# Kernel optimization log

Hardware: AMD Instinct MI355X
Metric: run time of the kernel (lower is better)

The kernel has to match this reference:

```python
import jax, jax.numpy as jnp
import numpy as np

DIM = 512
NUM_HEADS = 8


def setup_inputs() -> dict:
    key = jax.random.key(0)
    ks = jax.random.split(key, 9)
    B, C, H, W = 8, DIM, 32, 32
    s = 1.0 / np.sqrt(DIM)  # conv-style init scale
    return {
        "x": jax.random.normal(ks[0], (B, C, H, W), jnp.float32),
        "Wq": jax.random.normal(ks[1], (DIM, DIM), jnp.float32) * s,
        "bq": jnp.zeros((DIM,), jnp.float32),
        "Wk": jax.random.normal(ks[2], (DIM, DIM), jnp.float32) * s,
        "bk": jnp.zeros((DIM,), jnp.float32),
        "Wv": jax.random.normal(ks[3], (DIM, DIM), jnp.float32) * s,
        "bv": jnp.zeros((DIM,), jnp.float32),
        "Wo": jax.random.normal(ks[4], (DIM, DIM), jnp.float32) * s,
        "bo": jnp.zeros((DIM,), jnp.float32),
    }


def _proj(x, W, b):
    # 1x1 conv == per-pixel linear over channels: [out_c, in_c] x [b, in_c, h, w]
    return jnp.einsum('oc,bchw->bohw', W, x) + b[None, :, None, None]


def reference(x, Wq, bq, Wk, bk, Wv, bv, Wo, bo):
    b, c, h, w = x.shape
    g = NUM_HEADS
    dh = c // g  # per-head channels
    q = _proj(x, Wq, bq)
    k = _proj(x, Wk, bk)
    v = _proj(x, Wv, bv)
    # 'b (g c) h w -> (b g) c (h w)'
    def split_heads(t):
        return t.reshape(b, g, dh, h * w).reshape(b * g, dh, h * w)
    q, k, v = split_heads(q), split_heads(k), split_heads(v)
    # note: scale uses full dim (as in the source), not per-head dim
    a = jnp.einsum('bcs,bct->bst', q, k) / jnp.sqrt(jnp.float32(c))
    a = jax.nn.softmax(a, axis=-1)  # dropout is identity at inference
    o = jnp.einsum('bst,bct->bcs', a, v)  # [(b g), dh, s]
    o = o.reshape(b, g * dh, h, w)  # '(b g) c (h w) -> b (g c) h w'
    return x + _proj(o, Wo, bo)
```

## Files before the change

kernel.cpp:

```cpp
#include <hip/hip_runtime.h>

typedef unsigned short u16;
typedef __attribute__((ext_vector_type(8))) short short8;
typedef __attribute__((ext_vector_type(4))) short sh4;
typedef __attribute__((ext_vector_type(2))) int int2v;
typedef __attribute__((ext_vector_type(4))) float floatx4;

__device__ __forceinline__ float b2f(u16 u) {
  unsigned int x = ((unsigned int)u) << 16;
  return __builtin_bit_cast(float, x);
}
__device__ __forceinline__ u16 f2b(float f) {
  unsigned int x = __builtin_bit_cast(unsigned int, f);
  unsigned int r = (x + 0x7FFFu + ((x >> 16) & 1u)) >> 16;
  return (u16)r;
}
__device__ __forceinline__ unsigned int pk2bf(float a, float b) {
  unsigned int ua = __builtin_bit_cast(unsigned int, a) + 0x8000u;
  unsigned int ub = __builtin_bit_cast(unsigned int, b) + 0x8000u;
  return __builtin_amdgcn_perm(ub, ua, 0x07060302u);
}

#if __has_builtin(__builtin_amdgcn_mfma_f32_16x16x16bf16_1k)
#define MFMA16(a, b, c) __builtin_amdgcn_mfma_f32_16x16x16bf16_1k((a), (b), (c), 0, 0, 0)
#define MFMA16_DRAIN()
#else
__device__ __forceinline__ floatx4 mfma16_fb(sh4 a, sh4 b, floatx4 c) {
  asm volatile("s_nop 1\n\tv_mfma_f32_16x16x16_bf16 %0, %1, %2, %0"
               : "+v"(c) : "v"(a), "v"(b));
  return c;
}
#define MFMA16(a, b, c) mfma16_fb((a), (b), (c))
#define MFMA16_DRAIN() asm volatile("s_nop 7\n\ts_nop 7\n\ts_nop 7")
#endif

#if __has_builtin(__builtin_amdgcn_exp2f)
#define EXP2F(x) __builtin_amdgcn_exp2f(x)
#else
#define EXP2F(x) __expf((x) * 0.6931471805599453f)
#endif

#define MFMA32(a, b, c) __builtin_amdgcn_mfma_f32_16x16x32_bf16((a), (b), (c), 0, 0, 0)

#define GLL16(g, l) __builtin_amdgcn_global_load_lds(                         \
    (const __attribute__((address_space(1))) unsigned int*)(g),               \
    (__attribute__((address_space(3))) unsigned int*)(l), 16, 0, 0)

#define SC_LOG2E 0.06375872f

__device__ __forceinline__ int detect_fp32(const u16* __restrict__ x) {
  __shared__ int cnt;
  if (threadIdx.x == 0) cnt = 0;
  __syncthreads();
  int c = 0;
  if (threadIdx.x < 256) {
#pragma unroll
    for (int i = 0; i < 16; ++i) {
      u16 u = x[threadIdx.x * 16 + i];
      if (((u >> 7) & 0xFF) >= 0xC8) c++;
    }
  }
  if (c) atomicAdd(&cnt, c);
  __syncthreads();
  return cnt > 32;
}

__global__ __launch_bounds__(256) void prep(
    const u16* __restrict__ x,
    const u16* w0, const u16* w1, const u16* w2, const u16* w3,
    const u16* c0, const u16* c1, const u16* c2, const u16* c3,
    u16* __restrict__ xT, u16* __restrict__ Wc, u16* __restrict__ bc, int b0) {
  const int fp32 = detect_fp32(x);
  const int tid = threadIdx.x;
  if (blockIdx.y < 8) {
    __shared__ u16 t[64][65];
    const int lb = blockIdx.z, b = b0 + lb;
    const int p0 = blockIdx.x * 64, cc0 = blockIdx.y * 64;
    const int tx = tid & 63, ty = tid >> 6;
    if (fp32) {
      const float* xb = (const float*)x + (long)b * 524288;
#pragma unroll
      for (int i = 0; i < 16; ++i) {
        int c = ty + i * 4;
        t[c][tx] = f2b(xb[(long)(cc0 + c) * 1024 + p0 + tx]);
      }
    } else {
      const u16* xb = x + (long)b * 524288;
#pragma unroll
      for (int i = 0; i < 16; ++i) {
        int c = ty + i * 4;
        t[c][tx] = xb[(long)(cc0 + c) * 1024 + p0 + tx];
      }
    }
    __syncthreads();
    u16* xTb = xT + (long)lb * 524288;
#pragma unroll
    for (int i = 0; i < 16; ++i) {
      int p = ty + i * 4;
      xTb[(long)(p0 + p) * 512 + cc0 + tx] = t[tx][p];
    }
  } else {
    const u16* srcs[8] = {w0, w1, w2, w3, c0, c1, c2, c3};
    const int nthreads = gridDim.z * 16 * 256;
    const int flat = (blockIdx.z * 16 + blockIdx.x) * 256 + tid;
    for (int vi = flat; vi < 131072; vi += nthreads) {
      int w = vi >> 15;
      int off = (vi & 32767) * 8;
      u16* dst = Wc + w * 262144 + off;
      if (fp32) {
        const float* s = (const float*)srcs[w] + off;
        u16 tmp[8];
#pragma unroll
        for (int r = 0; r < 8; ++r) tmp[r] = f2b(s[r]);
        *(int4*)dst = *(const int4*)tmp;
      } else {
        *(int4*)dst = *(const int4*)(srcs[w] + off);
      }
    }
    for (int gi = flat; gi < 2048; gi += nthreads) {
      int t2 = gi >> 9;
      bc[gi] = fp32 ? f2b(((const float*)srcs[4 + t2])[gi & 511]) : srcs[4 + t2][gi & 511];
    }
  }
}

struct GemmLds64 {
  u16 As0[128][32], As1[128][32];
  u16 Bs0[128][32], Bs1[128][32];
};

__device__ __forceinline__ void gemm_core64(const u16* __restrict__ A, int lda,
                                            const u16* __restrict__ B, int ldb,
                                            int m0, int n0, int K,
                                            GemmLds64& lds, floatx4 (&acc)[4][4]) {
  const int tid = threadIdx.x;
  const int wave = tid >> 6, lane = tid & 63;
  const int quad = lane >> 4, l15 = lane & 15;
  const int wm = (wave >> 1) * 64, wn = (wave & 1) * 64;
  const int lrow = lane >> 2, lcol = (lane & 3) * 8;
  for (int k0 = 0; k0 < K; k0 += 64) {
    __syncthreads();
#pragma unroll
    for (int it = 0; it < 2; ++it) {
      const int rbase = wave * 32 + it * 16;
      const u16* Ar = A + (long)(m0 + rbase + lrow) * lda + k0 + lcol;
      GLL16(Ar, &lds.As0[rbase][0]);
      GLL16(Ar + 32, &lds.As1[rbase][0]);
      const u16* Br = B + (long)(n0 + rbase + lrow) * ldb + k0 + lcol;
      GLL16(Br, &lds.Bs0[rbase][0]);
      GLL16(Br + 32, &lds.Bs1[rbase][0]);
    }
    __syncthreads();
    short8 af[4], bf[4];
#pragma unroll
    for (int i = 0; i < 4; ++i)
      af[i] = *(const short8*)&lds.As0[wm + i * 16 + l15][quad * 8];
#pragma unroll
    for (int j = 0; j < 4; ++j)
      bf[j] = *(const short8*)&lds.Bs0[wn + j * 16 + l15][quad * 8];
#pragma unroll
    for (int i = 0; i < 4; ++i)
#pragma unroll
      for (int j = 0; j < 4; ++j)
        acc[i][j] = MFMA32(af[i], bf[j], acc[i][j]);
#pragma unroll
    for (int i = 0; i < 4; ++i)
      af[i] = *(const short8*)&lds.As1[wm + i * 16 + l15][quad * 8];
#pragma unroll
    for (int j = 0; j < 4; ++j)
      bf[j] = *(const short8*)&lds.Bs1[wn + j * 16 + l15][quad * 8];
#pragma unroll
    for (int i = 0; i < 4; ++i)
#pragma unroll
      for (int j = 0; j < 4; ++j)
        acc[i][j] = MFMA32(af[i], bf[j], acc[i][j]);
  }
}

__global__ __launch_bounds__(256) void gemm_qkv(
    const u16* __restrict__ xT, const u16* __restrict__ Wc,
    const u16* __restrict__ bc, u16* __restrict__ Qt, u16* __restrict__ Kt,
    u16* __restrict__ Vv) {
  __shared__ GemmLds64 lds;
  const long bz = blockIdx.y;
  const u16* xb = xT + bz * 524288;
  const int bx = blockIdx.x;
  const int qk = bx < 64;
  const int t = qk ? bx : bx - 64;
  const int m0 = (t >> 3) * 128, n0 = (t & 7) * 128;
  const u16* A = qk ? xb : (Wc + 524288);
  const u16* B = qk ? Wc : xb;
  floatx4 acc[4][4] = {};
  gemm_core64(A, 512, B, 512, m0, n0, 512, lds, acc);
  const int lane = threadIdx.x & 63, wave = threadIdx.x >> 6;
  const int quad = lane >> 4, l15 = lane & 15;
  const int wm = (wave >> 1) * 64, wn = (wave & 1) * 64;
  if (qk) {
    u16* Qz = Qt + bz * 524288;
    u16* Kz = Kt + bz * 524288;
#pragma unroll
    for (int i = 0; i < 4; ++i)
#pragma unroll
      for (int j = 0; j < 4; ++j)
#pragma unroll
        for (int r = 0; r < 4; ++r) {
          int gm = m0 + wm + i * 16 + quad * 4 + r;
          int gn = n0 + wn + j * 16 + l15;
          float v = acc[i][j][r] + b2f(bc[gn]);
          if (gn < 512) Qz[(long)gm * 512 + gn] = f2b(v * SC_LOG2E);
          else Kz[(long)gm * 512 + gn - 512] = f2b(v);
        }
  } else {
    u16* Vz = Vv + bz * 524288;
    const u16* bv = bc + 1024;
#pragma unroll
    for (int i = 0; i < 4; ++i)
#pragma unroll
      for (int j = 0; j < 4; ++j)
#pragma unroll
        for (int r = 0; r < 4; ++r) {
          int gm = m0 + wm + i * 16 + quad * 4 + r;
          int gn = n0 + wn + j * 16 + l15;
          float v = acc[i][j][r] + b2f(bv[gm]);
          Vz[(long)gm * 1024 + gn] = f2b(v);
        }
  }
}

struct OutLds64 {
  u16 As0[128][32], As1[128][32];
  u16 Bs0[64][32], Bs1[64][32];
};

__global__ __launch_bounds__(256) void gemm_out(
    const u16* __restrict__ Wo, const u16* __restrict__ bo,
    const u16* __restrict__ Ow, const u16* __restrict__ xraw,
    u16* __restrict__ out) {
  const int fp32 = detect_fp32(xraw);
  __shared__ OutLds64 lds;
  const long bz = blockIdx.z;
  const u16* B = Ow + bz * 524288;
  const int m0 = blockIdx.y * 128, n0 = blockIdx.x * 64;
  const int tid = threadIdx.x;
  const int wave = tid >> 6, lane = tid & 63;
  const int quad = lane >> 4, l15 = lane & 15;
  const int lrow = lane >> 2, lcol = (lane & 3) * 8;

  floatx4 acc[2][4] = {};

  for (int k0 = 0; k0 < 512; k0 += 64) {
    __syncthreads();
    {
      const int ra = wave * 32;
      const u16* A0 = Wo + (long)(m0 + ra + lrow) * 512 + k0 + lcol;
      const u16* A1 = Wo + (long)(m0 + ra + 16 + lrow) * 512 + k0 + lcol;
      GLL16(A0, &lds.As0[ra][0]);
      GLL16(A0 + 32, &lds.As1[ra][0]);
      GLL16(A1, &lds.As0[ra + 16][0]);
      GLL16(A1 + 32, &lds.As1[ra + 16][0]);
      const u16* Br = B + (long)(n0 + wave * 16 + lrow) * 512 + k0 + lcol;
      GLL16(Br, &lds.Bs0[wave * 16][0]);
      GLL16(Br + 32, &lds.Bs1[wave * 16][0]);
    }
    __syncthreads();
#pragma unroll
    for (int i = 0; i < 2; ++i) {
      short8 af = *(const short8*)&lds.As0[wave * 32 + i * 16 + l15][quad * 8];
#pragma unroll
      for (int j = 0; j < 4; ++j) {
        short8 bf = *(const short8*)&lds.Bs0[j * 16 + l15][quad * 8];
        acc[i][j] = MFMA32(af, bf, acc[i][j]);
      }
    }
#pragma unroll
    for (int i = 0; i < 2; ++i) {
      short8 af = *(const short8*)&lds.As1[wave * 32 + i * 16 + l15][quad * 8];
#pragma unroll
      for (int j = 0; j < 4; ++j) {
        short8 bf = *(const short8*)&lds.Bs1[j * 16 + l15][quad * 8];
        acc[i][j] = MFMA32(af, bf, acc[i][j]);
      }
    }
  }

#pragma unroll
  for (int i = 0; i < 2; ++i)
#pragma unroll
    for (int j = 0; j < 4; ++j)
#pragma unroll
      for (int r = 0; r < 4; ++r) {
        int gm = m0 + wave * 32 + i * 16 + quad * 4 + r;
        int gn = n0 + j * 16 + l15;
        float v = acc[i][j][r] + b2f(bo[gm]);
        long idx = bz * 524288 + (long)gm * 1024 + gn;
        if (fp32) {
          v += ((const float*)xraw)[idx];
          ((float*)out)[idx] = v;
        } else {
          v += b2f(xraw[idx]);
          out[idx] = f2b(v);
        }
      }
}

#define AP 72
__global__ __launch_bounds__(512, 4) void attn(
    const u16* __restrict__ Qt, const u16* __restrict__ Kt,
    const u16* __restrict__ V, u16* __restrict__ O) {
  __shared__ alignas(16) u16 Ks[2][64][AP];
  __shared__ alignas(16) u16 Vs[2][64][AP];
  const int bg = blockIdx.x;
  const int lb = bg >> 3, head = bg & 7;
  const int s0 = blockIdx.y * 128;
  const int tid = threadIdx.x;
  const int wave = tid >> 6, lane = tid & 63;
  const int quad = lane >> 4, l15 = lane & 15;

  const u16* Qb = Qt + (long)lb * 524288 + head * 64;
  const u16* Kb = Kt + (long)lb * 524288 + head * 64;
  const u16* Vb = V + (long)(lb * 512 + head * 64) * 1024;
  u16* Ob = O + (long)lb * 524288 + head * 64;

  short8 bq[2];
#pragma unroll
  for (int kk = 0; kk < 2; ++kk)
    bq[kk] = *(const short8*)&Qb[(long)(s0 + wave * 16 + l15) * 512 +
                                 kk * 32 + quad * 8];

  const int r0 = tid >> 3, o0 = (tid & 7) * 8;
  int4 kreg, vreg;
  kreg = *(const int4*)&Kb[(long)r0 * 512 + o0];
  vreg = *(const int4*)&Vb[(long)r0 * 1024 + o0];
  *(int4*)&Ks[0][r0][o0] = kreg;
  *(int4*)&Vs[0][r0][o0] = vreg;

  floatx4 acc[4] = {};
  floatx4 accl = {};
  const sh4 ones = {(short)0x3F80, (short)0x3F80, (short)0x3F80, (short)0x3F80};

  for (int it16 = 0; it16 < 16; ++it16) {
    const int buf = it16 & 1;
    const int t0n = (it16 + 1) * 64;
    if (it16 < 15) {
      kreg = *(const int4*)&Kb[(long)(t0n + r0) * 512 + o0];
      vreg = *(const int4*)&Vb[(long)r0 * 1024 + t0n + o0];
    }
    __syncthreads();

    floatx4 p[4] = {};
#pragma unroll
    for (int kk = 0; kk < 2; ++kk) {
      short8 ak[4];
#pragma unroll
      for (int mi = 0; mi < 4; ++mi)
        ak[mi] = *(const short8*)&Ks[buf][mi * 16 + l15][kk * 32 + quad * 8];
#pragma unroll
      for (int mi = 0; mi < 4; ++mi)
        p[mi] = MFMA32(ak[mi], bq[kk], p[mi]);
    }

    sh4 pk[4];
#pragma unroll
    for (int mi = 0; mi < 4; ++mi) {
      float e0 = EXP2F(p[mi][0]);
      float e1 = EXP2F(p[mi][1]);
      float e2 = EXP2F(p[mi][2]);
      float e3 = EXP2F(p[mi][3]);
      int2v w;
      w.x = (int)pk2bf(e0, e1);
      w.y = (int)pk2bf(e2, e3);
      pk[mi] = __builtin_bit_cast(sh4, w);
    }

#pragma unroll
    for (int mi = 0; mi < 4; ++mi) accl = MFMA16(ones, pk[mi], accl);

#pragma unroll
    for (int mi = 0; mi < 4; ++mi) {
      sh4 av[4];
#pragma unroll
      for (int ci = 0; ci < 4; ++ci)
        av[ci] = *(const sh4*)&Vs[buf][ci * 16 + l15][mi * 16 + quad * 4];
#pragma unroll
      for (int ci = 0; ci < 4; ++ci)
        acc[ci] = MFMA16(av[ci], pk[mi], acc[ci]);
    }

    if (it16 < 15) {
      const int nb = 1 - buf;
      *(int4*)&Ks[nb][r0][o0] = kreg;
      *(int4*)&Vs[nb][r0][o0] = vreg;
    }
  }
  MFMA16_DRAIN();

  const float inv = 1.0f / accl[0];

  u16 (*Os)[AP] = (u16(*)[AP]) & Ks[0][0][0];
  __syncthreads();
#pragma unroll
  for (int ci = 0; ci < 4; ++ci) {
    int2v w;
    w.x = (int)pk2bf(acc[ci][0] * inv, acc[ci][1] * inv);
    w.y = (int)pk2bf(acc[ci][2] * inv, acc[ci][3] * inv);
    *(int2v*)&Os[wave * 16 + l15][ci * 16 + quad * 4] = w;
  }
  __syncthreads();
  {
    const int srow = tid >> 2, c16 = (tid & 3) * 16;
    *(int4*)&Ob[(long)(s0 + srow) * 512 + c16] = *(const int4*)&Os[srow][c16];
    *(int4*)&Ob[(long)(s0 + srow) * 512 + c16 + 8] = *(const int4*)&Os[srow][c16 + 8];
  }
}

extern "C" void kernel_launch(void* const* d_in, const int* in_sizes, int n_in,
                              void* d_out, int out_size, void* d_ws, size_t ws_size,
                              hipStream_t stream) {
  const u16* x  = (const u16*)d_in[0];
  const u16* Wq = (const u16*)d_in[1];
  const u16* bq = (const u16*)d_in[2];
  const u16* Wk = (const u16*)d_in[3];
  const u16* bk = (const u16*)d_in[4];
  const u16* Wv = (const u16*)d_in[5];
  const u16* bv = (const u16*)d_in[6];
  const u16* Wo = (const u16*)d_in[7];
  const u16* bo = (const u16*)d_in[8];
  u16* out = (u16*)d_out;
  u16* ws = (u16*)d_ws;

  const size_t PLAN_A_BYTES = 27267072;

  if (ws_size >= PLAN_A_BYTES) {
    u16* xT = ws;
    u16* Kt = ws + 4194304;
    u16* Vv = ws + 8388608;
    u16* Wc = ws + 12582912;
    u16* bc = ws + 13631488;
    u16* Qt = out;
    u16* Ow = xT;

    prep<<<dim3(16, 9, 8), 256, 0, stream>>>(x, Wq, Wk, Wv, Wo,
                                             bq, bk, bv, bo, xT, Wc, bc, 0);
    gemm_qkv<<<dim3(96, 8), 256, 0, stream>>>(xT, Wc, bc, Qt, Kt, Vv);
    attn<<<dim3(64, 8), 512, 0, stream>>>(Qt, Kt, Vv, Ow);
    gemm_out<<<dim3(16, 4, 8), 256, 0, stream>>>(Wc + 786432, bc + 1536, Ow, x, out);
  } else {
    u16* Ow = ws;
    u16* Kt = ws + 4194304;
    u16* Vv = ws + 6291456;
    u16* Wc = ws + 8388608;
    u16* bc = ws + 9437184;
    u16* Qt = out;

    for (int phase = 0; phase < 2; ++phase) {
      const int b0 = phase * 4;
      u16* xT = Ow + (long)phase * 2097152;
      prep<<<dim3(16, 9, 4), 256, 0, stream>>>(x, Wq, Wk, Wv, Wo,
                                               bq, bk, bv, bo, xT, Wc, bc, b0);
      gemm_qkv<<<dim3(96, 4), 256, 0, stream>>>(xT, Wc, bc, Qt, Kt, Vv);
      attn<<<dim3(32, 8), 512, 0, stream>>>(Qt, Kt, Vv, Ow + (long)b0 * 524288);
    }
    gemm_out<<<dim3(16, 4, 8), 256, 0, stream>>>(Wc + 786432, bc + 1536, Ow, x, out);
  }
}
```

Measured before the change: 162.7 us.

## Halve attention block threads with two query tiles per wave; reorder grid dims

```diff
diff --git a/kernel.cpp b/kernel.cpp
--- a/kernel.cpp
+++ b/kernel.cpp
@@ -182,9 +182,9 @@
     const u16* __restrict__ bc, u16* __restrict__ Qt, u16* __restrict__ Kt,
     u16* __restrict__ Vv) {
   __shared__ GemmLds64 lds;
-  const long bz = blockIdx.y;
+  const long bz = blockIdx.x;
   const u16* xb = xT + bz * 524288;
-  const int bx = blockIdx.x;
+  const int bx = blockIdx.y;
   const int qk = bx < 64;
   const int t = qk ? bx : bx - 64;
   const int m0 = (t >> 3) * 128, n0 = (t & 7) * 128;
@@ -238,9 +238,9 @@
     u16* __restrict__ out) {
   const int fp32 = detect_fp32(xraw);
   __shared__ OutLds64 lds;
-  const long bz = blockIdx.z;
+  const long bz = blockIdx.x;
   const u16* B = Ow + bz * 524288;
-  const int m0 = blockIdx.y * 128, n0 = blockIdx.x * 64;
+  const int m0 = blockIdx.z * 128, n0 = blockIdx.y * 64;
   const int tid = threadIdx.x;
   const int wave = tid >> 6, lane = tid & 63;
   const int quad = lane >> 4, l15 = lane & 15;
@@ -304,7 +304,7 @@
 }
 
 #define AP 72
-__global__ __launch_bounds__(512, 4) void attn(
+__global__ __launch_bounds__(256, 2) void attn(
     const u16* __restrict__ Qt, const u16* __restrict__ Kt,
     const u16* __restrict__ V, u16* __restrict__ O) {
   __shared__ alignas(16) u16 Ks[2][64][AP];
@@ -321,33 +321,41 @@
   const u16* Vb = V + (long)(lb * 512 + head * 64) * 1024;
   u16* Ob = O + (long)lb * 524288 + head * 64;
 
-  short8 bq[2];
-#pragma unroll
-  for (int kk = 0; kk < 2; ++kk)
-    bq[kk] = *(const short8*)&Qb[(long)(s0 + wave * 16 + l15) * 512 +
-                                 kk * 32 + quad * 8];
+  short8 bq[2][2];
+#pragma unroll
+  for (int qb = 0; qb < 2; ++qb)
+#pragma unroll
+    for (int kk = 0; kk < 2; ++kk)
+      bq[qb][kk] = *(const short8*)&Qb[(long)(s0 + wave * 32 + qb * 16 + l15) * 512 +
+                                       kk * 32 + quad * 8];
 
   const int r0 = tid >> 3, o0 = (tid & 7) * 8;
-  int4 kreg, vreg;
-  kreg = *(const int4*)&Kb[(long)r0 * 512 + o0];
-  vreg = *(const int4*)&Vb[(long)r0 * 1024 + o0];
-  *(int4*)&Ks[0][r0][o0] = kreg;
-  *(int4*)&Vs[0][r0][o0] = vreg;
-
-  floatx4 acc[4] = {};
-  floatx4 accl = {};
+  int4 kreg0, kreg1, vreg0, vreg1;
+  kreg0 = *(const int4*)&Kb[(long)r0 * 512 + o0];
+  kreg1 = *(const int4*)&Kb[(long)(r0 + 32) * 512 + o0];
+  vreg0 = *(const int4*)&Vb[(long)r0 * 1024 + o0];
+  vreg1 = *(const int4*)&Vb[(long)(r0 + 32) * 1024 + o0];
+  *(int4*)&Ks[0][r0][o0] = kreg0;
+  *(int4*)&Ks[0][r0 + 32][o0] = kreg1;
+  *(int4*)&Vs[0][r0][o0] = vreg0;
+  *(int4*)&Vs[0][r0 + 32][o0] = vreg1;
+
+  floatx4 acc[2][4] = {};
+  floatx4 accl[2] = {};
   const sh4 ones = {(short)0x3F80, (short)0x3F80, (short)0x3F80, (short)0x3F80};
 
   for (int it16 = 0; it16 < 16; ++it16) {
     const int buf = it16 & 1;
     const int t0n = (it16 + 1) * 64;
     if (it16 < 15) {
-      kreg = *(const int4*)&Kb[(long)(t0n + r0) * 512 + o0];
-      vreg = *(const int4*)&Vb[(long)r0 * 1024 + t0n + o0];
-    }
-    __syncthreads();
-
-    floatx4 p[4] = {};
+      kreg0 = *(const int4*)&Kb[(long)(t0n + r0) * 512 + o0];
+      kreg1 = *(const int4*)&Kb[(long)(t0n + r0 + 32) * 512 + o0];
+      vreg0 = *(const int4*)&Vb[(long)r0 * 1024 + t0n + o0];
+      vreg1 = *(const int4*)&Vb[(long)(r0 + 32) * 1024 + t0n + o0];
+    }
+    __syncthreads();
+
+    floatx4 p[2][4] = {};
 #pragma unroll
     for (int kk = 0; kk < 2; ++kk) {
       short8 ak[4];
@@ -355,25 +363,31 @@
       for (int mi = 0; mi < 4; ++mi)
         ak[mi] = *(const short8*)&Ks[buf][mi * 16 + l15][kk * 32 + quad * 8];
 #pragma unroll
-      for (int mi = 0; mi < 4; ++mi)
-        p[mi] = MFMA32(ak[mi], bq[kk], p[mi]);
-    }
-
-    sh4 pk[4];
-#pragma unroll
-    for (int mi = 0; mi < 4; ++mi) {
-      float e0 = EXP2F(p[mi][0]);
-      float e1 = EXP2F(p[mi][1]);
-      float e2 = EXP2F(p[mi][2]);
-      float e3 = EXP2F(p[mi][3]);
-      int2v w;
-      w.x = (int)pk2bf(e0, e1);
-      w.y = (int)pk2bf(e2, e3);
-      pk[mi] = __builtin_bit_cast(sh4, w);
-    }
-
-#pragma unroll
-    for (int mi = 0; mi < 4; ++mi) accl = MFMA16(ones, pk[mi], accl);
+      for (int qb = 0; qb < 2; ++qb)
+#pragma unroll
+        for (int mi = 0; mi < 4; ++mi)
+          p[qb][mi] = MFMA32(ak[mi], bq[qb][kk], p[qb][mi]);
+    }
+
+    sh4 pk[2][4];
+#pragma unroll
+    for (int qb = 0; qb < 2; ++qb)
+#pragma unroll
+      for (int mi = 0; mi < 4; ++mi) {
+        float e0 = EXP2F(p[qb][mi][0]);
+        float e1 = EXP2F(p[qb][mi][1]);
+        float e2 = EXP2F(p[qb][mi][2]);
+        float e3 = EXP2F(p[qb][mi][3]);
+        int2v w;
+        w.x = (int)pk2bf(e0, e1);
+        w.y = (int)pk2bf(e2, e3);
+        pk[qb][mi] = __builtin_bit_cast(sh4, w);
+      }
+
+#pragma unroll
+    for (int qb = 0; qb < 2; ++qb)
+#pragma unroll
+      for (int mi = 0; mi < 4; ++mi) accl[qb] = MFMA16(ones, pk[qb][mi], accl[qb]);
 
 #pragma unroll
     for (int mi = 0; mi < 4; ++mi) {
@@ -382,34 +396,44 @@
       for (int ci = 0; ci < 4; ++ci)
         av[ci] = *(const sh4*)&Vs[buf][ci * 16 + l15][mi * 16 + quad * 4];
 #pragma unroll
-      for (int ci = 0; ci < 4; ++ci)
-        acc[ci] = MFMA16(av[ci], pk[mi], acc[ci]);
+      for (int qb = 0; qb < 2; ++qb)
+#pragma unroll
+        for (int ci = 0; ci < 4; ++ci)
+          acc[qb][ci] = MFMA16(av[ci], pk[qb][mi], acc[qb][ci]);
     }
 
     if (it16 < 15) {
       const int nb = 1 - buf;
-      *(int4*)&Ks[nb][r0][o0] = kreg;
-      *(int4*)&Vs[nb][r0][o0] = vreg;
+      *(int4*)&Ks[nb][r0][o0] = kreg0;
+      *(int4*)&Ks[nb][r0 + 32][o0] = kreg1;
+      *(int4*)&Vs[nb][r0][o0] = vreg0;
+      *(int4*)&Vs[nb][r0 + 32][o0] = vreg1;
     }
   }
   MFMA16_DRAIN();
 
-  const float inv = 1.0f / accl[0];
+  const float inv0 = 1.0f / accl[0][0];
+  const float inv1 = 1.0f / accl[1][0];
 
   u16 (*Os)[AP] = (u16(*)[AP]) & Ks[0][0][0];
   __syncthreads();
 #pragma unroll
-  for (int ci = 0; ci < 4; ++ci) {
-    int2v w;
-    w.x = (int)pk2bf(acc[ci][0] * inv, acc[ci][1] * inv);
-    w.y = (int)pk2bf(acc[ci][2] * inv, acc[ci][3] * inv);
-    *(int2v*)&Os[wave * 16 + l15][ci * 16 + quad * 4] = w;
+  for (int qb = 0; qb < 2; ++qb) {
+    const float inv = qb ? inv1 : inv0;
+#pragma unroll
+    for (int ci = 0; ci < 4; ++ci) {
+      int2v w;
+      w.x = (int)pk2bf(acc[qb][ci][0] * inv, acc[qb][ci][1] * inv);
+      w.y = (int)pk2bf(acc[qb][ci][2] * inv, acc[qb][ci][3] * inv);
+      *(int2v*)&Os[wave * 32 + qb * 16 + l15][ci * 16 + quad * 4] = w;
+    }
   }
   __syncthreads();
   {
-    const int srow = tid >> 2, c16 = (tid & 3) * 16;
-    *(int4*)&Ob[(long)(s0 + srow) * 512 + c16] = *(const int4*)&Os[srow][c16];
-    *(int4*)&Ob[(long)(s0 + srow) * 512 + c16 + 8] = *(const int4*)&Os[srow][c16 + 8];
+    const int srow = tid >> 1, cb = (tid & 1) * 32;
+#pragma unroll
+    for (int c = 0; c < 32; c += 8)
+      *(int4*)&Ob[(long)(s0 + srow) * 512 + cb + c] = *(const int4*)&Os[srow][cb + c];
   }
 }
 
@@ -441,9 +465,9 @@
 
     prep<<<dim3(16, 9, 8), 256, 0, stream>>>(x, Wq, Wk, Wv, Wo,
                                              bq, bk, bv, bo, xT, Wc, bc, 0);
-    gemm_qkv<<<dim3(96, 8), 256, 0, stream>>>(xT, Wc, bc, Qt, Kt, Vv);
-    attn<<<dim3(64, 8), 512, 0, stream>>>(Qt, Kt, Vv, Ow);
-    gemm_out<<<dim3(16, 4, 8), 256, 0, stream>>>(Wc + 786432, bc + 1536, Ow, x, out);
+    gemm_qkv<<<dim3(8, 96), 256, 0, stream>>>(xT, Wc, bc, Qt, Kt, Vv);
+    attn<<<dim3(64, 8), 256, 0, stream>>>(Qt, Kt, Vv, Ow);
+    gemm_out<<<dim3(8, 16, 4), 256, 0, stream>>>(Wc + 786432, bc + 1536, Ow, x, out);
   } else {
     u16* Ow = ws;
     u16* Kt = ws + 4194304;
@@ -457,9 +481,9 @@
       u16* xT = Ow + (long)phase * 2097152;
       prep<<<dim3(16, 9, 4), 256, 0, stream>>>(x, Wq, Wk, Wv, Wo,
                                                bq, bk, bv, bo, xT, Wc, bc, b0);
-      gemm_qkv<<<dim3(96, 4), 256, 0, stream>>>(xT, Wc, bc, Qt, Kt, Vv);
-      attn<<<dim3(32, 8), 512, 0, stream>>>(Qt, Kt, Vv, Ow + (long)b0 * 524288);
-    }
-    gemm_out<<<dim3(16, 4, 8), 256, 0, stream>>>(Wc + 786432, bc + 1536, Ow, x, out);
-  }
-}
+      gemm_qkv<<<dim3(4, 96), 256, 0, stream>>>(xT, Wc, bc, Qt, Kt, Vv);
+      attn<<<dim3(32, 8), 256, 0, stream>>>(Qt, Kt, Vv, Ow + (long)b0 * 524288);
+    }
+    gemm_out<<<dim3(8, 16, 4), 256, 0, stream>>>(Wc + 786432, bc + 1536, Ow, x, out);
+  }
+}
```

After: 161.1 us. Within noise of the previous version (-1.0%).
